# Optimization experiments

Measured on AMD Instinct MI355X. Metric: run time of the kernel, lower is better.

Reference implementation:

```python
import jax, jax.numpy as jnp
import numpy as np

NODE_DIM = 256
EDGE_DIM = 64
TIME_DIM = 1024
HEADS = 8
HEAD_DIM = NODE_DIM // HEADS
MLP = 2
BS, N = 32, 48
BN = BS * N
E = BS * N * (N - 1)


def _lin(k, fin, fout):
    return jax.random.normal(k, (fin, fout), dtype=jnp.float32) / np.sqrt(fin)


def _edge_index():
    idx = np.arange(N)
    src, dst = np.meshgrid(idx, idx, indexing='ij')
    m = src != dst
    src, dst = src[m], dst[m]              # [N*(N-1)] per graph
    offs = (np.arange(BS) * N)[:, None]
    row = (offs + src[None, :]).reshape(-1)
    col = (offs + dst[None, :]).reshape(-1)
    return jnp.asarray(np.stack([row, col]), dtype=jnp.int32)


def setup_inputs() -> dict:
    key = jax.random.key(0)
    ks = jax.random.split(key, 32)
    d = {
        'pos': jax.random.normal(ks[0], (BN, 3), jnp.float32),
        'h': jax.random.normal(ks[1], (BN, NODE_DIM), jnp.float32),
        'edge_attr': jax.random.normal(ks[2], (E, EDGE_DIM), jnp.float32),
        'node_mask': jnp.ones((BN, 1), jnp.float32),
        'node_time_emb': jax.random.normal(ks[3], (BN, TIME_DIM), jnp.float32),
        'edge_time_emb': jax.random.normal(ks[4], (E, TIME_DIM), jnp.float32),
        'edge_index': _edge_index(),
        # edge_emb: Linear(edge_dim+1 -> edge_dim)
        'W_ee': _lin(ks[5], EDGE_DIM + 1, EDGE_DIM), 'b_ee': jnp.zeros((EDGE_DIM,)),
        # AdaLN time MLPs (SiLU -> Linear)
        'W_nt': _lin(ks[6], TIME_DIM, 6 * NODE_DIM), 'b_nt': jnp.zeros((6 * NODE_DIM,)),
        'W_et': _lin(ks[7], TIME_DIM, 6 * EDGE_DIM), 'b_et': jnp.zeros((6 * EDGE_DIM,)),
        # Trans_Layer sparse attention
        'Wq': _lin(ks[8], NODE_DIM, NODE_DIM), 'bq': jnp.zeros((NODE_DIM,)),
        'Wk': _lin(ks[9], NODE_DIM, NODE_DIM), 'bk': jnp.zeros((NODE_DIM,)),
        'Wv': _lin(ks[10], NODE_DIM, NODE_DIM), 'bv': jnp.zeros((NODE_DIM,)),
        'We0': _lin(ks[11], EDGE_DIM, NODE_DIM),
        'We1': _lin(ks[12], EDGE_DIM, NODE_DIM),
        'W_n2e': _lin(ks[13], NODE_DIM, EDGE_DIM), 'b_n2e': jnp.zeros((EDGE_DIM,)),
        # node FFN
        'W_ff1': _lin(ks[14], NODE_DIM, MLP * NODE_DIM), 'b_ff1': jnp.zeros((MLP * NODE_DIM,)),
        'W_ff2': _lin(ks[15], MLP * NODE_DIM, NODE_DIM), 'b_ff2': jnp.zeros((NODE_DIM,)),
        # edge FFN
        'W_ff3': _lin(ks[16], EDGE_DIM, MLP * EDGE_DIM), 'b_ff3': jnp.zeros((MLP * EDGE_DIM,)),
        'W_ff4': _lin(ks[17], MLP * EDGE_DIM, EDGE_DIM), 'b_ff4': jnp.zeros((EDGE_DIM,)),
        # CondEquiUpdate
        'coors_scale': jnp.full((1,), 0.01, jnp.float32),
        'W_ut': _lin(ks[18], TIME_DIM, 2 * NODE_DIM), 'b_ut': jnp.zeros((2 * NODE_DIM,)),
        'W_ui': _lin(ks[19], 2 * NODE_DIM + EDGE_DIM + 1, NODE_DIM), 'b_ui': jnp.zeros((NODE_DIM,)),
        'W_uc1': _lin(ks[20], NODE_DIM, NODE_DIM), 'b_uc1': jnp.zeros((NODE_DIM,)),
        'W_uc2': _lin(ks[21], NODE_DIM, 1),
    }
    return d


def _ln(x):  # LayerNorm, no affine, eps=1e-6
    m = x.mean(-1, keepdims=True)
    v = ((x - m) ** 2).mean(-1, keepdims=True)
    return (x - m) * jax.lax.rsqrt(v + 1e-6)


def _modulate(x, shift, scale):
    return x * (1 + scale) + shift


def _block(pos, h, edge_attr, node_mask, node_time_emb, edge_time_emb, edge_index,
           W_ee, b_ee, W_nt, b_nt, W_et, b_et, Wq, bq, Wk, bk, Wv, bv, We0, We1,
           W_n2e, b_n2e, W_ff1, b_ff1, W_ff2, b_ff2, W_ff3, b_ff3, W_ff4, b_ff4,
           coors_scale, W_ut, b_ut, W_ui, b_ui, W_uc1, b_uc1, W_uc2):
    row, col = edge_index[0], edge_index[1]  # row = source j, col = target i
    diff = pos[row] - pos[col]                              # [E,3]
    dist = jnp.sqrt(jnp.sum(diff * diff, -1, keepdims=True) + 1e-12)  # [E,1]
    ea = jnp.concatenate([dist, edge_attr], -1) @ W_ee + b_ee

    nt = jax.nn.silu(node_time_emb) @ W_nt + b_nt
    n_sh_msa, n_sc_msa, n_g_msa, n_sh_mlp, n_sc_mlp, n_g_mlp = jnp.split(nt, 6, axis=1)
    et = jax.nn.silu(edge_time_emb) @ W_et + b_et
    e_sh_msa, e_sc_msa, e_g_msa, e_sh_mlp, e_sc_mlp, e_g_mlp = jnp.split(et, 6, axis=1)

    hh = _modulate(_ln(h), n_sh_msa, n_sc_msa)
    ea = _modulate(_ln(ea), e_sh_msa, e_sc_msa)

    # sparse multi-head attention over edges (Trans_Layer)
    q = (hh @ Wq + bq).reshape(BN, HEADS, HEAD_DIM)
    k = (hh @ Wk + bk).reshape(BN, HEADS, HEAD_DIM)
    v = (hh @ Wv + bv).reshape(BN, HEADS, HEAD_DIM)
    e0 = (ea @ We0).reshape(E, HEADS, HEAD_DIM)
    e1 = (ea @ We1).reshape(E, HEADS, HEAD_DIM)
    alpha = jnp.sum(q[col] * k[row] * e0, -1) / np.sqrt(HEAD_DIM)  # [E,H]
    mx = jax.ops.segment_max(alpha, col, num_segments=BN)
    ex = jnp.exp(alpha - mx[col])
    den = jax.ops.segment_sum(ex, col, num_segments=BN)
    att = ex / (den[col] + 1e-16)
    msg = v[row] * e1 * att[:, :, None]
    h_node = jax.ops.segment_sum(msg, col, num_segments=BN).reshape(BN, NODE_DIM)

    h_edge = (h_node[row] + h_node[col]) @ W_n2e + b_n2e

    h_node = h + n_g_msa * h_node
    h_node = _modulate(_ln(h_node), n_sh_mlp, n_sc_mlp) * node_mask
    ff = jax.nn.silu(h_node @ W_ff1 + b_ff1) @ W_ff2 + b_ff2
    h_out = (h_node + n_g_mlp * ff) * node_mask

    h_e = edge_attr + e_g_msa * h_edge
    h_e = _modulate(_ln(h_e), e_sh_mlp, e_sc_mlp)
    ffe = jax.nn.silu(h_e @ W_ff3 + b_ff3) @ W_ff4 + b_ff4
    h_edge_out = h_e + e_g_mlp * ffe

    # CondEquiUpdate: equivariant coordinate update
    h_input = jnp.concatenate([h_out[row], h_out[col], h_edge_out, dist], -1)
    nrm = jnp.linalg.norm(diff, axis=-1, keepdims=True)
    cdiff = diff / jnp.clip(nrm, 1e-8) * coors_scale        # CoorsNorm(scale_init=0.01)
    t_shift, t_scale = jnp.split(jax.nn.silu(edge_time_emb) @ W_ut + b_ut, 2, axis=1)
    inv = _modulate(_ln(h_input @ W_ui + b_ui), t_shift, t_scale)
    inv = jnp.tanh(jax.nn.silu(inv @ W_uc1 + b_uc1) @ W_uc2)  # [E,1]
    trans = cdiff * inv
    pos_out = pos + jax.ops.segment_sum(trans, row, num_segments=BN)
    return h_out, h_edge_out, pos_out


def reference(pos, h, edge_attr, node_mask, node_time_emb, edge_time_emb, edge_index,
              W_ee, b_ee, W_nt, b_nt, W_et, b_et, Wq, bq, Wk, bk, Wv, bv, We0, We1,
              W_n2e, b_n2e, W_ff1, b_ff1, W_ff2, b_ff2, W_ff3, b_ff3, W_ff4, b_ff4,
              coors_scale, W_ut, b_ut, W_ui, b_ui, W_uc1, b_uc1, W_uc2):
    return _block(pos, h, edge_attr, node_mask, node_time_emb, edge_time_emb, edge_index,
                  W_ee, b_ee, W_nt, b_nt, W_et, b_et, Wq, bq, Wk, bk, Wv, bv, We0, We1,
                  W_n2e, b_n2e, W_ff1, b_ff1, W_ff2, b_ff2, W_ff3, b_ff3, W_ff4, b_ff4,
                  coors_scale, W_ut, b_ut, W_ui, b_ui, W_uc1, b_uc1, W_uc2)
```

## Files before the change

kernel.cpp:

```cpp
#include <hip/hip_runtime.h>

typedef unsigned short u16;
typedef __attribute__((ext_vector_type(4))) u16 u16x4;
typedef __attribute__((ext_vector_type(8))) u16 u16x8;
typedef __attribute__((ext_vector_type(8))) short s16x8;
typedef __attribute__((ext_vector_type(4))) float f32x4;

#define E_CNT 72192
#define BN_CNT 1536
#define EPG 2256

__device__ __forceinline__ float b2f(u16 u) {
    union { unsigned int i; float f; } x; x.i = ((unsigned int)u) << 16; return x.f;
}
__device__ __forceinline__ u16 f2b(float f) {
    union { float f; unsigned int i; } x; x.f = f;
    unsigned int r = x.i + 0x7fffu + ((x.i >> 16) & 1u);
    return (u16)(r >> 16);
}
__device__ __forceinline__ float siluf(float x) { return x / (1.f + expf(-x)); }

__device__ __forceinline__ void gll16(const void* g, void* l) {
    __builtin_amdgcn_global_load_lds(
        (const __attribute__((address_space(1))) void*)g,
        (__attribute__((address_space(3))) void*)l, 16, 0, 0);
}

__device__ __forceinline__ float wave_ln64(float x) {
    float s = x;
    #pragma unroll
    for (int off = 1; off < 64; off <<= 1) s += __shfl_xor(s, off);
    float mean = s * 0.015625f;
    float d = x - mean;
    float v2 = d * d;
    #pragma unroll
    for (int off = 1; off < 64; off <<= 1) v2 += __shfl_xor(v2, off);
    return d * rsqrtf(v2 * 0.015625f + 1e-6f);
}

__device__ __forceinline__ float block_ln256(float x) {
    __shared__ float tmp[4];
    int t = threadIdx.x;
    float s = x;
    #pragma unroll
    for (int off = 1; off < 64; off <<= 1) s += __shfl_xor(s, off);
    if ((t & 63) == 0) tmp[t >> 6] = s;
    __syncthreads();
    float mean = (tmp[0] + tmp[1] + tmp[2] + tmp[3]) * (1.f / 256.f);
    float d = x - mean;
    float v2 = d * d;
    #pragma unroll
    for (int off = 1; off < 64; off <<= 1) v2 += __shfl_xor(v2, off);
    __syncthreads();
    if ((t & 63) == 0) tmp[t >> 6] = v2;
    __syncthreads();
    float var = (tmp[0] + tmp[1] + tmp[2] + tmp[3]) * (1.f / 256.f);
    return d * rsqrtf(var + 1e-6f);
}

template<int ACT, int OUTBF>
__global__ __launch_bounds__(256) void k_gemm(
    const u16* __restrict__ A, const u16* __restrict__ Bt,
    const float* __restrict__ bias, void* __restrict__ C,
    int M, int N, int K)
{
    __shared__ u16 As[64][40];
    __shared__ u16 Bs[64][40];
    int bn0 = blockIdx.x * 64, bm0 = blockIdx.y * 64;
    int t = threadIdx.x;
    int lane = t & 63, wave = t >> 6;
    int wm = wave >> 1, wn = wave & 1;
    int lr = t >> 2, lc = (t & 3) * 8;
    f32x4 acc[2][2] = {};
    const u16* Ap = A + (size_t)(bm0 + lr) * K + lc;
    const u16* Bp = Bt + (size_t)(bn0 + lr) * K + lc;
    int fr = lane & 15, fk = (lane >> 4) * 8;
    for (int k0 = 0; k0 < K; k0 += 32) {
        *(u16x8*)&As[lr][lc] = *(const u16x8*)(Ap + k0);
        *(u16x8*)&Bs[lr][lc] = *(const u16x8*)(Bp + k0);
        __syncthreads();
        s16x8 a0 = *(const s16x8*)&As[wm * 32 + fr][fk];
        s16x8 a1 = *(const s16x8*)&As[wm * 32 + 16 + fr][fk];
        s16x8 b0 = *(const s16x8*)&Bs[wn * 32 + fr][fk];
        s16x8 b1 = *(const s16x8*)&Bs[wn * 32 + 16 + fr][fk];
        acc[0][0] = __builtin_amdgcn_mfma_f32_16x16x32_bf16(a0, b0, acc[0][0], 0, 0, 0);
        acc[0][1] = __builtin_amdgcn_mfma_f32_16x16x32_bf16(a0, b1, acc[0][1], 0, 0, 0);
        acc[1][0] = __builtin_amdgcn_mfma_f32_16x16x32_bf16(a1, b0, acc[1][0], 0, 0, 0);
        acc[1][1] = __builtin_amdgcn_mfma_f32_16x16x32_bf16(a1, b1, acc[1][1], 0, 0, 0);
        __syncthreads();
    }
    int cIn = lane & 15, r4 = (lane >> 4) * 4;
    #pragma unroll
    for (int i = 0; i < 2; i++)
    #pragma unroll
    for (int j = 0; j < 2; j++) {
        int col = bn0 + wn * 32 + j * 16 + cIn;
        float bv = bias ? bias[col] : 0.f;
        #pragma unroll
        for (int r = 0; r < 4; r++) {
            int rowg = bm0 + wm * 32 + i * 16 + r4 + r;
            float vv = acc[i][j][r] + bv;
            if (ACT == 1) vv = siluf(vv);
            if (OUTBF) ((u16*)C)[(size_t)rowg * N + col] = f2b(vv);
            else       ((float*)C)[(size_t)rowg * N + col] = vv;
        }
    }
}

template<int ACT, int OUTBF>
__global__ __launch_bounds__(256) void k_gemm128(
    const u16* __restrict__ A, const u16* __restrict__ Bt,
    const float* __restrict__ bias, void* __restrict__ C,
    int M, int N, int K)
{
    __shared__ u16 As[3][128 * 32];
    __shared__ u16 Bs[3][128 * 32];
    const int t = threadIdx.x;
    const int lane = t & 63, wv = t >> 6;
    const int wm = wv >> 1, wn = wv & 1;
    const int nwg = gridDim.x * gridDim.y;
    const int orig = blockIdx.y * gridDim.x + blockIdx.x;
    const int q8 = nwg >> 3, r8 = nwg & 7;
    const int xcd = orig & 7, lin = orig >> 3;
    const int wgid = (xcd < r8 ? xcd * (q8 + 1) : r8 * (q8 + 1) + (xcd - r8) * q8) + lin;
    const int bxs = wgid % gridDim.x, bys = wgid / gridDim.x;
    const int bn0 = bxs * 128, bm0 = bys * 128;
    const int srow = t >> 2;
    const int scol = ((t & 3) ^ ((t >> 3) & 3)) * 8;
    const u16* Ap = A + (size_t)(bm0 + srow) * K + scol;
    const u16* Bp = Bt + (size_t)(bn0 + srow) * K + scol;
    const size_t rstep = (size_t)64 * K;
    const int woff = wv * 16 * 32;
    const int fr = lane & 15;
    const int fkc = (((lane >> 4) ^ ((fr >> 1) & 3)) * 8);
    f32x4 acc[4][4] = {};
    const int NT = K >> 5;

    auto STAGE = [&](int b, int ko) {
        gll16(Ap + ko, &As[b][woff]);
        gll16(Ap + ko + rstep, &As[b][woff + 64 * 32]);
        gll16(Bp + ko, &Bs[b][woff]);
        gll16(Bp + ko + rstep, &Bs[b][woff + 64 * 32]);
    };
    auto COMPUTE = [&](int b) {
        const u16* aBase = &As[b][wm * 64 * 32];
        const u16* bBase = &Bs[b][wn * 64 * 32];
        s16x8 af[4], bfr[4];
        #pragma unroll
        for (int m = 0; m < 4; m++) af[m] = *(const s16x8*)&aBase[(m * 16 + fr) * 32 + fkc];
        #pragma unroll
        for (int n = 0; n < 4; n++) bfr[n] = *(const s16x8*)&bBase[(n * 16 + fr) * 32 + fkc];
        #pragma unroll
        for (int m = 0; m < 4; m++)
        #pragma unroll
        for (int n = 0; n < 4; n++)
            acc[m][n] = __builtin_amdgcn_mfma_f32_16x16x32_bf16(af[m], bfr[n], acc[m][n], 0, 0, 0);
    };

    STAGE(0, 0);
    if (NT > 1) STAGE(1, 32);
    int cur = 0;
    for (int tt = 0; tt < NT; tt++) {
        if (tt + 2 < NT) STAGE((cur + 2) % 3, (tt + 2) * 32);
        __builtin_amdgcn_sched_barrier(0);
        int ahead = NT - 1 - tt; if (ahead > 2) ahead = 2;
        if (ahead == 2)      asm volatile("s_waitcnt vmcnt(8)" ::: "memory");
        else if (ahead == 1) asm volatile("s_waitcnt vmcnt(4)" ::: "memory");
        else                 asm volatile("s_waitcnt vmcnt(0)" ::: "memory");
        __builtin_amdgcn_sched_barrier(0);
        __builtin_amdgcn_s_barrier();
        COMPUTE(cur);
        __builtin_amdgcn_s_barrier();
        __builtin_amdgcn_sched_barrier(0);
        cur = (cur + 1) % 3;
    }

    const int cIn = lane & 15, r4 = (lane >> 4) * 4;
    #pragma unroll
    for (int n = 0; n < 4; n++) {
        int col = bn0 + wn * 64 + n * 16 + cIn;
        float bv = bias ? bias[col] : 0.f;
        #pragma unroll
        for (int m = 0; m < 4; m++) {
            #pragma unroll
            for (int r = 0; r < 4; r++) {
                int rowg = bm0 + wm * 64 + m * 16 + r4 + r;
                float vv = acc[m][n][r] + bv;
                if (ACT == 1) vv = siluf(vv);
                if (OUTBF) ((u16*)C)[(size_t)rowg * N + col] = f2b(vv);
                else       ((float*)C)[(size_t)rowg * N + col] = vv;
            }
        }
    }
}

struct ConvJob { const float* W; u16* Wt; int ldw, k0, n0, K, nc_start; };
struct CopyJob { const float* src; float* dst; int n; };
struct BatchArgs { ConvJob cj[17]; CopyJob cp[5]; int conv_blocks; };

__global__ __launch_bounds__(256) void k_prep(BatchArgs a)
{
    int b = blockIdx.x;
    if (b < a.conv_blocks) {
        int j = 0;
        #pragma unroll 1
        while (j + 1 < 17 && a.cj[j + 1].nc_start <= b) ++j;
        const ConvJob J = a.cj[j];
        int n = b - J.nc_start;
        for (int k = threadIdx.x; k < J.K; k += 256)
            J.Wt[(size_t)n * J.K + k] = f2b(J.W[(size_t)(J.k0 + k) * J.ldw + J.n0 + n]);
    } else {
        int c = b - a.conv_blocks;
        const CopyJob C = a.cp[c];
        for (int i = threadIdx.x; i < C.n; i += 256) C.dst[i] = C.src[i];
    }
}

__global__ void k_silu_bf(const float* __restrict__ in, u16* __restrict__ out, int n4)
{
    int i = blockIdx.x * 256 + threadIdx.x;
    int stride = gridDim.x * 256;
    for (; i < n4; i += stride) {
        f32x4 v = *(const f32x4*)(in + (size_t)i * 4);
        u16x4 o;
        #pragma unroll
        for (int j = 0; j < 4; j++) o[j] = f2b(siluf(v[j]));
        *(u16x4*)(out + (size_t)i * 4) = o;
    }
}

__global__ __launch_bounds__(256) void k_edge_pre(
    const float* __restrict__ pos, const float* __restrict__ edge_attr,
    const int* __restrict__ ei, const float* __restrict__ W_ee,
    const float* __restrict__ b_ee, const float* __restrict__ coors_scale,
    const u16* __restrict__ etf,
    u16* __restrict__ ea_mod, float* __restrict__ dist, float* __restrict__ cdiff)
{
    __shared__ float Ws[65][64];
    int t = threadIdx.x;
    for (int i = t; i < 65 * 64; i += 256) Ws[i >> 6][i & 63] = W_ee[i];
    __syncthreads();
    int l = t & 63;
    float bee = b_ee[l];
    float cscale = coors_scale[0];
    for (int g = 0; g < 16; g++) {
        int e = blockIdx.x * 64 + g * 4 + (t >> 6);
        int row = ei[e], col = ei[E_CNT + e];
        float d0 = pos[row * 3 + 0] - pos[col * 3 + 0];
        float d1 = pos[row * 3 + 1] - pos[col * 3 + 1];
        float d2 = pos[row * 3 + 2] - pos[col * 3 + 2];
        float ssq = d0 * d0 + d1 * d1 + d2 * d2;
        float dst = sqrtf(ssq + 1e-12f);
        float nrm = sqrtf(ssq);
        float cs = cscale / fmaxf(nrm, 1e-8f);
        if (l == 0) {
            dist[e] = dst;
            cdiff[e * 3 + 0] = d0 * cs; cdiff[e * 3 + 1] = d1 * cs; cdiff[e * 3 + 2] = d2 * cs;
        }
        float attr = edge_attr[(size_t)e * 64 + l];
        float acc = dst * Ws[0][l];
        for (int f = 0; f < 64; f++) acc += __shfl(attr, f) * Ws[1 + f][l];
        acc += bee;
        float y = wave_ln64(acc);
        const u16* ep = etf + (size_t)e * 896;
        float m = y * (1.f + b2f(ep[64 + l])) + b2f(ep[l]);
        ea_mod[(size_t)e * 64 + l] = f2b(m);
    }
}

__global__ __launch_bounds__(256) void k_node_hh(
    const float* __restrict__ h, const float* __restrict__ nt, u16* __restrict__ hh)
{
    int n = blockIdx.x, c = threadIdx.x;
    float x = h[(size_t)n * 256 + c];
    float y = block_ln256(x);
    float m = y * (1.f + nt[(size_t)n * 1536 + 256 + c]) + nt[(size_t)n * 1536 + c];
    hh[(size_t)n * 256 + c] = f2b(m);
}

__global__ __launch_bounds__(256) void k_agg(
    const float* __restrict__ qkv, const u16* __restrict__ e01,
    float* __restrict__ hnode, u16* __restrict__ hnode_bf)
{
    int n = blockIdx.x;
    int b = n / 48, i = n % 48;
    int t = threadIdx.x;
    __shared__ float qs[8][33];
    __shared__ float att[47][8];
    __shared__ float mxs[8], dens[8];
    __shared__ int elist[47], slist[47];
    qs[t >> 5][t & 31] = qkv[(size_t)n * 768 + t];
    if (t < 47) {
        int s = t + (t >= i ? 1 : 0);
        slist[t] = s;
        elist[t] = b * EPG + s * 47 + (i < s ? i : i - 1);
    }
    __syncthreads();
    for (int idx = t; idx < 376; idx += 256) {
        int j = idx >> 3, hh = idx & 7;
        int src = b * 48 + slist[j];
        int e = elist[j];
        const float* kp = qkv + (size_t)src * 768 + 256 + hh * 32;
        const u16* ep = e01 + (size_t)e * 512 + hh * 32;
        float p = 0.f;
        #pragma unroll
        for (int d = 0; d < 32; d++) p += qs[hh][d] * kp[d] * b2f(ep[d]);
        att[j][hh] = p * 0.17677669529663687f;
    }
    __syncthreads();
    if (t < 8) {
        float m = -1e30f;
        for (int j = 0; j < 47; j++) m = fmaxf(m, att[j][t]);
        float den = 0.f;
        for (int j = 0; j < 47; j++) den += expf(att[j][t] - m);
        mxs[t] = m; dens[t] = den + 1e-16f;
    }
    __syncthreads();
    for (int idx = t; idx < 376; idx += 256) {
        int j = idx >> 3, hh = idx & 7;
        att[j][hh] = expf(att[j][hh] - mxs[hh]) / dens[hh];
    }
    __syncthreads();
    int c = t, hh = t >> 5;
    float acc = 0.f;
    for (int j = 0; j < 47; j++) {
        int src = b * 48 + slist[j];
        int e = elist[j];
        acc += att[j][hh] * qkv[(size_t)src * 768 + 512 + c] * b2f(e01[(size_t)e * 512 + 256 + c]);
    }
    hnode[(size_t)n * 256 + c] = acc;
    hnode_bf[(size_t)n * 256 + c] = f2b(acc);
}

__global__ __launch_bounds__(256) void k_node_mod(
    const float* __restrict__ h, const float* __restrict__ hnode_raw,
    const float* __restrict__ nt, const float* __restrict__ mask,
    float* __restrict__ hmod, u16* __restrict__ hmod_bf)
{
    int n = blockIdx.x, c = threadIdx.x;
    float x = h[(size_t)n * 256 + c] + nt[(size_t)n * 1536 + 512 + c] * hnode_raw[(size_t)n * 256 + c];
    float y = block_ln256(x);
    float m = (y * (1.f + nt[(size_t)n * 1536 + 1024 + c]) + nt[(size_t)n * 1536 + 768 + c]) * mask[n];
    hmod[(size_t)n * 256 + c] = m;
    hmod_bf[(size_t)n * 256 + c] = f2b(m);
}

__global__ void k_hout(const float* __restrict__ hmod, const float* __restrict__ ff2,
                       const float* __restrict__ nt, const float* __restrict__ mask,
                       float* __restrict__ out, u16* __restrict__ hout_bf)
{
    int i = blockIdx.x * 256 + threadIdx.x;
    if (i >= BN_CNT * 256) return;
    int n = i >> 8, c = i & 255;
    float v = (hmod[i] + nt[(size_t)n * 1536 + 1280 + c] * ff2[i]) * mask[n];
    out[i] = v;
    hout_bf[i] = f2b(v);
}

__global__ __launch_bounds__(256) void k_edge_mod(
    const float* __restrict__ Q1, const float* __restrict__ b_n2e,
    const float* __restrict__ edge_attr, const int* __restrict__ ei,
    const u16* __restrict__ etf, float* __restrict__ hemod, u16* __restrict__ hemod_bf)
{
    int e = blockIdx.x * 4 + (threadIdx.x >> 6);
    int l = threadIdx.x & 63;
    int row = ei[e], col = ei[E_CNT + e];
    float hedge = Q1[(size_t)row * 64 + l] + Q1[(size_t)col * 64 + l] + b_n2e[l];
    const u16* ep = etf + (size_t)e * 896;
    float x = edge_attr[(size_t)e * 64 + l] + b2f(ep[128 + l]) * hedge;
    float y = wave_ln64(x);
    float m = y * (1.f + b2f(ep[256 + l])) + b2f(ep[192 + l]);
    hemod[(size_t)e * 64 + l] = m;
    hemod_bf[(size_t)e * 64 + l] = f2b(m);
}

__global__ void k_edge_out(const float* __restrict__ hemod, const float* __restrict__ ff4,
                           const u16* __restrict__ etf,
                           float* __restrict__ out2, u16* __restrict__ heout_bf)
{
    size_t i = (size_t)blockIdx.x * 256 + threadIdx.x;
    if (i >= (size_t)E_CNT * 64) return;
    int e = (int)(i >> 6), c = (int)(i & 63);
    float v = hemod[i] + b2f(etf[(size_t)e * 896 + 320 + c]) * ff4[i];
    out2[i] = v;
    heout_bf[i] = f2b(v);
}

__global__ __launch_bounds__(256) void k_inv_pre(
    const float* __restrict__ p12,
    const u16* __restrict__ P3, const float* __restrict__ dist,
    const float* __restrict__ W_ui, const float* __restrict__ b_ui,
    const int* __restrict__ ei, const u16* __restrict__ etf, u16* __restrict__ invmod)
{
    int e = blockIdx.x, c = threadIdx.x;
    int row = ei[e], col = ei[E_CNT + e];
    float x = p12[(size_t)row * 512 + c] + p12[(size_t)col * 512 + 256 + c]
            + b2f(P3[(size_t)e * 256 + c]) + dist[e] * W_ui[576 * 256 + c] + b_ui[c];
    float y = block_ln256(x);
    const u16* ep = etf + (size_t)e * 896;
    float m = y * (1.f + b2f(ep[640 + c])) + b2f(ep[384 + c]);
    invmod[(size_t)e * 256 + c] = f2b(m);
}

__global__ __launch_bounds__(256) void k_inv(const u16* __restrict__ uc1,
                                             const float* __restrict__ W_uc2,
                                             float* __restrict__ inv)
{
    int e = blockIdx.x * 4 + (threadIdx.x >> 6);
    int l = threadIdx.x & 63;
    u16x4 v = *(const u16x4*)(uc1 + (size_t)e * 256 + l * 4);
    const float* w = W_uc2 + l * 4;
    float s = b2f(v[0]) * w[0] + b2f(v[1]) * w[1] + b2f(v[2]) * w[2] + b2f(v[3]) * w[3];
    #pragma unroll
    for (int off = 1; off < 64; off <<= 1) s += __shfl_xor(s, off);
    if (l == 0) inv[e] = tanhf(s);
}

__global__ void k_pos(const float* __restrict__ pos, const float* __restrict__ cdiff,
                      const float* __restrict__ inv, float* __restrict__ out3)
{
    int n = blockIdx.x * 256 + threadIdx.x;
    if (n >= BN_CNT) return;
    int b = n / 48, s = n % 48;
    int e0 = b * EPG + s * 47;
    float a0 = 0.f, a1 = 0.f, a2 = 0.f;
    for (int j = 0; j < 47; j++) {
        float f = inv[e0 + j];
        a0 += cdiff[(size_t)(e0 + j) * 3 + 0] * f;
        a1 += cdiff[(size_t)(e0 + j) * 3 + 1] * f;
        a2 += cdiff[(size_t)(e0 + j) * 3 + 2] * f;
    }
    out3[n * 3 + 0] = pos[n * 3 + 0] + a0;
    out3[n * 3 + 1] = pos[n * 3 + 1] + a1;
    out3[n * 3 + 2] = pos[n * 3 + 2] + a2;
}

extern "C" void kernel_launch(void* const* d_in, const int* in_sizes, int n_in,
                              void* d_out, int out_size, void* d_ws, size_t ws_size,
                              hipStream_t stream)
{
    (void)in_sizes; (void)n_in; (void)out_size; (void)ws_size;
    const float* pos       = (const float*)d_in[0];
    const float* h         = (const float*)d_in[1];
    const float* edge_attr = (const float*)d_in[2];
    const float* node_mask = (const float*)d_in[3];
    const float* nte       = (const float*)d_in[4];
    const float* ete       = (const float*)d_in[5];
    const int*   ei        = (const int*)d_in[6];
    const float* W_ee = (const float*)d_in[7];  const float* b_ee = (const float*)d_in[8];
    const float* W_nt = (const float*)d_in[9];  const float* b_nt = (const float*)d_in[10];
    const float* W_et = (const float*)d_in[11]; const float* b_et = (const float*)d_in[12];
    const float* Wq  = (const float*)d_in[13];  const float* bq  = (const float*)d_in[14];
    const float* Wk  = (const float*)d_in[15];  const float* bk  = (const float*)d_in[16];
    const float* Wv  = (const float*)d_in[17];  const float* bv  = (const float*)d_in[18];
    const float* We0 = (const float*)d_in[19];  const float* We1 = (const float*)d_in[20];
    const float* W_n2e = (const float*)d_in[21]; const float* b_n2e = (const float*)d_in[22];
    const float* W_ff1 = (const float*)d_in[23]; const float* b_ff1 = (const float*)d_in[24];
    const float* W_ff2 = (const float*)d_in[25]; const float* b_ff2 = (const float*)d_in[26];
    const float* W_ff3 = (const float*)d_in[27]; const float* b_ff3 = (const float*)d_in[28];
    const float* W_ff4 = (const float*)d_in[29]; const float* b_ff4 = (const float*)d_in[30];
    const float* coors_scale = (const float*)d_in[31];
    const float* W_ut = (const float*)d_in[32]; const float* b_ut = (const float*)d_in[33];
    const float* W_ui = (const float*)d_in[34]; const float* b_ui = (const float*)d_in[35];
    const float* W_uc1 = (const float*)d_in[36]; const float* b_uc1 = (const float*)d_in[37];
    const float* W_uc2 = (const float*)d_in[38];

    const size_t E = E_CNT;
    char* ws = (char*)d_ws;
    size_t off = 0;
    auto AL = [&](size_t b) { size_t o = off; off += (b + 255) & ~(size_t)255; return o; };

    size_t o_wtcat  = AL(896 * 1024 * 2);
    size_t o_wtnt   = AL(1536 * 1024 * 2);
    size_t o_wtqkv  = AL(768 * 256 * 2);
    size_t o_wte01  = AL(512 * 64 * 2);
    size_t o_wtn2e  = AL(64 * 256 * 2);
    size_t o_wtff1  = AL(512 * 256 * 2), o_wtff2 = AL(256 * 512 * 2);
    size_t o_wtff3  = AL(128 * 64 * 2),  o_wtff4 = AL(64 * 128 * 2);
    size_t o_wtuiab = AL(512 * 256 * 2);
    size_t o_wtuic  = AL(256 * 64 * 2),  o_wtuc1 = AL(256 * 256 * 2);
    size_t o_bias896 = AL(896 * 4);
    size_t o_bias768 = AL(768 * 4);
    size_t o_reg1 = AL(E * 1024 * 2);
    size_t o_etf  = AL(E * 896 * 2);
    size_t o_ntes = AL(1536 * 1024 * 2);
    size_t o_ntf  = AL((size_t)1536 * 1536 * 4);
    size_t o_eamod = AL(E * 64 * 2);
    size_t o_dist = AL(E * 4), o_cdiff = AL(E * 12);
    size_t o_qkv  = AL(1536 * 768 * 4);
    size_t o_reg3 = AL(E * 512 * 2);
    size_t o_hnode = AL(1536 * 256 * 4), o_hnodebf = AL(1536 * 256 * 2);
    size_t o_q1 = AL(1536 * 64 * 4);
    size_t o_hh = AL(1536 * 256 * 2);
    size_t o_hmod = AL(1536 * 256 * 4), o_hmodbf = AL(1536 * 256 * 2);
    size_t o_ff1 = AL(1536 * 512 * 2), o_ff2 = AL(1536 * 256 * 4);
    size_t o_houtbf = AL(1536 * 256 * 2);
    size_t o_hemod = AL(E * 64 * 4), o_hemodbf = AL(E * 64 * 2);
    size_t o_p12 = AL(1536 * 512 * 4);
    size_t o_inv = AL(E * 4);
    size_t o_etes = o_reg1;
    size_t o_p3 = o_reg1;
    size_t o_invmod = o_reg1 + E * 256 * 2;
    size_t o_uc1o = o_reg1 + E * 256 * 4;
    size_t o_e01 = o_reg3;
    size_t o_ffem = o_reg3;
    size_t o_ff4o = o_reg3 + E * 128 * 2;
    size_t o_heoutbf = o_reg3 + E * 128 * 2 + E * 64 * 4;

    #define WSU(o) ((u16*)(ws + (o)))
    #define WSF(o) ((float*)(ws + (o)))

    {
        BatchArgs a;
        int s = 0; int j = 0;
        auto add = [&](const float* W, u16* Wt, int ldw, int k0, int n0, int K, int NC) {
            a.cj[j++] = ConvJob{W, Wt, ldw, k0, n0, K, s}; s += NC;
        };
        add(W_et, WSU(o_wtcat), 384, 0, 0, 1024, 384);
        add(W_ut, WSU(o_wtcat) + (size_t)384 * 1024, 512, 0, 0, 1024, 512);
        add(W_nt, WSU(o_wtnt), 1536, 0, 0, 1024, 1536);
        add(Wq, WSU(o_wtqkv), 256, 0, 0, 256, 256);
        add(Wk, WSU(o_wtqkv) + (size_t)256 * 256, 256, 0, 0, 256, 256);
        add(Wv, WSU(o_wtqkv) + (size_t)512 * 256, 256, 0, 0, 256, 256);
        add(We0, WSU(o_wte01), 256, 0, 0, 64, 256);
        add(We1, WSU(o_wte01) + (size_t)256 * 64, 256, 0, 0, 64, 256);
        add(W_n2e, WSU(o_wtn2e), 64, 0, 0, 256, 64);
        add(W_ff1, WSU(o_wtff1), 512, 0, 0, 256, 512);
        add(W_ff2, WSU(o_wtff2), 256, 0, 0, 512, 256);
        add(W_ff3, WSU(o_wtff3), 128, 0, 0, 64, 128);
        add(W_ff4, WSU(o_wtff4), 64, 0, 0, 128, 64);
        add(W_ui, WSU(o_wtuiab), 256, 0, 0, 256, 256);
        add(W_ui, WSU(o_wtuiab) + (size_t)256 * 256, 256, 256, 0, 256, 256);
        add(W_ui, WSU(o_wtuic), 256, 512, 0, 64, 256);
        add(W_uc1, WSU(o_wtuc1), 256, 0, 0, 256, 256);
        a.conv_blocks = s;
        a.cp[0] = CopyJob{b_et, WSF(o_bias896), 384};
        a.cp[1] = CopyJob{b_ut, WSF(o_bias896) + 384, 512};
        a.cp[2] = CopyJob{bq, WSF(o_bias768), 256};
        a.cp[3] = CopyJob{bk, WSF(o_bias768) + 256, 256};
        a.cp[4] = CopyJob{bv, WSF(o_bias768) + 512, 256};
        k_prep<<<s + 5, 256, 0, stream>>>(a);
    }

    k_silu_bf<<<2048, 256, 0, stream>>>(ete, WSU(o_etes), (int)(E * 1024 / 4));
    k_silu_bf<<<1024, 256, 0, stream>>>(nte, WSU(o_ntes), 1536 * 1024 / 4);

    k_gemm128<0, 1><<<dim3(7, 564), 256, 0, stream>>>(WSU(o_etes), WSU(o_wtcat), WSF(o_bias896), WSU(o_etf), E_CNT, 896, 1024);
    k_gemm<0, 0><<<dim3(24, 24), 256, 0, stream>>>(WSU(o_ntes), WSU(o_wtnt), b_nt, WSF(o_ntf), 1536, 1536, 1024);

    k_edge_pre<<<1128, 256, 0, stream>>>(pos, edge_attr, ei, W_ee, b_ee, coors_scale,
                                         WSU(o_etf), WSU(o_eamod), WSF(o_dist), WSF(o_cdiff));

    k_node_hh<<<1536, 256, 0, stream>>>(h, WSF(o_ntf), WSU(o_hh));
    k_gemm<0, 0><<<dim3(12, 24), 256, 0, stream>>>(WSU(o_hh), WSU(o_wtqkv), WSF(o_bias768), WSF(o_qkv), 1536, 768, 256);
    k_gemm128<0, 1><<<dim3(4, 564), 256, 0, stream>>>(WSU(o_eamod), WSU(o_wte01), nullptr, WSU(o_e01), E_CNT, 512, 64);
    k_agg<<<1536, 256, 0, stream>>>(WSF(o_qkv), WSU(o_e01), WSF(o_hnode), WSU(o_hnodebf));

    k_gemm<0, 0><<<dim3(1, 24), 256, 0, stream>>>(WSU(o_hnodebf), WSU(o_wtn2e), nullptr, WSF(o_q1), 1536, 64, 256);

    k_node_mod<<<1536, 256, 0, stream>>>(h, WSF(o_hnode), WSF(o_ntf), node_mask, WSF(o_hmod), WSU(o_hmodbf));
    k_gemm<1, 1><<<dim3(8, 24), 256, 0, stream>>>(WSU(o_hmodbf), WSU(o_wtff1), b_ff1, WSU(o_ff1), 1536, 512, 256);
    k_gemm<0, 0><<<dim3(4, 24), 256, 0, stream>>>(WSU(o_ff1), WSU(o_wtff2), b_ff2, WSF(o_ff2), 1536, 256, 512);
    k_hout<<<1536, 256, 0, stream>>>(WSF(o_hmod), WSF(o_ff2), WSF(o_ntf), node_mask, (float*)d_out, WSU(o_houtbf));

    k_edge_mod<<<18048, 256, 0, stream>>>(WSF(o_q1), b_n2e, edge_attr, ei, WSU(o_etf), WSF(o_hemod), WSU(o_hemodbf));
    k_gemm128<1, 1><<<dim3(1, 564), 256, 0, stream>>>(WSU(o_hemodbf), WSU(o_wtff3), b_ff3, WSU(o_ffem), E_CNT, 128, 64);
    k_gemm<0, 0><<<dim3(1, 1128), 256, 0, stream>>>(WSU(o_ffem), WSU(o_wtff4), b_ff4, WSF(o_ff4o), E_CNT, 64, 128);
    k_edge_out<<<18048, 256, 0, stream>>>(WSF(o_hemod), WSF(o_ff4o), WSU(o_etf),
                                          (float*)d_out + 393216, WSU(o_heoutbf));

    k_gemm<0, 0><<<dim3(8, 24), 256, 0, stream>>>(WSU(o_houtbf), WSU(o_wtuiab), nullptr, WSF(o_p12), 1536, 512, 256);
    k_gemm128<0, 1><<<dim3(2, 564), 256, 0, stream>>>(WSU(o_heoutbf), WSU(o_wtuic), nullptr, WSU(o_p3), E_CNT, 256, 64);
    k_inv_pre<<<E_CNT, 256, 0, stream>>>(WSF(o_p12), WSU(o_p3), WSF(o_dist),
                                         W_ui, b_ui, ei, WSU(o_etf), WSU(o_invmod));
    k_gemm128<1, 1><<<dim3(2, 564), 256, 0, stream>>>(WSU(o_invmod), WSU(o_wtuc1), b_uc1, WSU(o_uc1o), E_CNT, 256, 256);
    k_inv<<<18048, 256, 0, stream>>>(WSU(o_uc1o), W_uc2, WSF(o_inv));
    k_pos<<<6, 256, 0, stream>>>(pos, WSF(o_cdiff), WSF(o_inv), (float*)d_out + 393216 + E_CNT * 64);

    #undef WSU
    #undef WSF
}
```

Measured before the change: 758.5 us.

## Add 256x256-tile GEMM kernel with 512 threads for large edge GEMMs

Adds a new bf16 MFMA GEMM kernel using 256x256 output tiles, 8 waves per block and a triple-buffered LDS pipeline. The four large edge-dimension GEMMs switch to it from the 128-tile kernel, which raises data reuse per block and cuts global traffic. For the N=896 GEMM the padded fourth column tile is masked on store, and the weight workspace is grown to 1024 rows so the out-of-range B loads stay in bounds. The larger tile uses about 96KB of LDS and many accumulator registers, so only one block fits per CU, and the N=896 case spends compute on the padded columns.

```diff
diff --git a/kernel.cpp b/kernel.cpp
--- a/kernel.cpp
+++ b/kernel.cpp
@@ -189,6 +189,95 @@
                 if (ACT == 1) vv = siluf(vv);
                 if (OUTBF) ((u16*)C)[(size_t)rowg * N + col] = f2b(vv);
                 else       ((float*)C)[(size_t)rowg * N + col] = vv;
+            }
+        }
+    }
+}
+
+template<int ACT, int OUTBF>
+__global__ __launch_bounds__(512, 1) void k_gemm256(
+    const u16* __restrict__ A, const u16* __restrict__ Bt,
+    const float* __restrict__ bias, void* __restrict__ C,
+    int M, int N, int K)
+{
+    __shared__ u16 As[3][256 * 32];
+    __shared__ u16 Bs[3][256 * 32];
+    const int t = threadIdx.x;
+    const int lane = t & 63, wv = t >> 6;
+    const int wm = wv >> 2, wn = wv & 3;
+    const int nwg = gridDim.x * gridDim.y;
+    const int orig = blockIdx.y * gridDim.x + blockIdx.x;
+    const int q8 = nwg >> 3, r8 = nwg & 7;
+    const int xcd = orig & 7, lin = orig >> 3;
+    const int wgid = (xcd < r8 ? xcd * (q8 + 1) : r8 * (q8 + 1) + (xcd - r8) * q8) + lin;
+    const int bn0 = (wgid % gridDim.x) * 256, bm0 = (wgid / gridDim.x) * 256;
+    const int r0 = t >> 2;
+    const int c0 = ((t & 3) ^ ((t >> 3) & 3)) * 8;
+    const u16* A0 = A + (size_t)(bm0 + r0) * K + c0;
+    const u16* B0 = Bt + (size_t)(bn0 + r0) * K + c0;
+    const size_t rstep = (size_t)128 * K;
+    const int w0 = (wv * 64) * 8;
+    const int w1 = (512 + wv * 64) * 8;
+    const int fr = lane & 15;
+    const int fkc = (((lane >> 4) ^ ((fr >> 1) & 3)) * 8);
+    f32x4 acc[8][4] = {};
+    const int NT = K >> 5;
+
+    auto STAGE = [&](int b, int ko) {
+        gll16(A0 + ko, &As[b][w0]);
+        gll16(A0 + ko + rstep, &As[b][w1]);
+        gll16(B0 + ko, &Bs[b][w0]);
+        gll16(B0 + ko + rstep, &Bs[b][w1]);
+    };
+    auto COMPUTE = [&](int b) {
+        s16x8 af[8], bfr[4];
+        #pragma unroll
+        for (int m = 0; m < 8; m++)
+            af[m] = *(const s16x8*)&As[b][(wm * 128 + m * 16 + fr) * 32 + fkc];
+        #pragma unroll
+        for (int n = 0; n < 4; n++)
+            bfr[n] = *(const s16x8*)&Bs[b][(wn * 64 + n * 16 + fr) * 32 + fkc];
+        #pragma unroll
+        for (int m = 0; m < 8; m++)
+        #pragma unroll
+        for (int n = 0; n < 4; n++)
+            acc[m][n] = __builtin_amdgcn_mfma_f32_16x16x32_bf16(af[m], bfr[n], acc[m][n], 0, 0, 0);
+    };
+
+    STAGE(0, 0);
+    if (NT > 1) STAGE(1, 32);
+    int cur = 0;
+    for (int tt = 0; tt < NT; tt++) {
+        if (tt + 2 < NT) STAGE((cur + 2) % 3, (tt + 2) * 32);
+        __builtin_amdgcn_sched_barrier(0);
+        int ahead = NT - 1 - tt; if (ahead > 2) ahead = 2;
+        if (ahead == 2)      asm volatile("s_waitcnt vmcnt(8)" ::: "memory");
+        else if (ahead == 1) asm volatile("s_waitcnt vmcnt(4)" ::: "memory");
+        else                 asm volatile("s_waitcnt vmcnt(0)" ::: "memory");
+        __builtin_amdgcn_sched_barrier(0);
+        __builtin_amdgcn_s_barrier();
+        COMPUTE(cur);
+        __builtin_amdgcn_s_barrier();
+        __builtin_amdgcn_sched_barrier(0);
+        cur = (cur + 1) % 3;
+    }
+
+    const int cIn = lane & 15, r4 = (lane >> 4) * 4;
+    #pragma unroll
+    for (int n = 0; n < 4; n++) {
+        int col = bn0 + wn * 64 + n * 16 + cIn;
+        if (col < N) {
+            float bv = bias ? bias[col] : 0.f;
+            #pragma unroll
+            for (int m = 0; m < 8; m++) {
+                #pragma unroll
+                for (int r = 0; r < 4; r++) {
+                    int rowg = bm0 + wm * 128 + m * 16 + r4 + r;
+                    float vv = acc[m][n][r] + bv;
+                    if (ACT == 1) vv = siluf(vv);
+                    if (OUTBF) ((u16*)C)[(size_t)rowg * N + col] = f2b(vv);
+                    else       ((float*)C)[(size_t)rowg * N + col] = vv;
+                }
             }
         }
     }
@@ -470,7 +559,7 @@
     size_t off = 0;
     auto AL = [&](size_t b) { size_t o = off; off += (b + 255) & ~(size_t)255; return o; };
 
-    size_t o_wtcat  = AL(896 * 1024 * 2);
+    size_t o_wtcat  = AL((size_t)1024 * 1024 * 2);
     size_t o_wtnt   = AL(1536 * 1024 * 2);
     size_t o_wtqkv  = AL(768 * 256 * 2);
     size_t o_wte01  = AL(512 * 64 * 2);
@@ -545,7 +634,8 @@
     k_silu_bf<<<2048, 256, 0, stream>>>(ete, WSU(o_etes), (int)(E * 1024 / 4));
     k_silu_bf<<<1024, 256, 0, stream>>>(nte, WSU(o_ntes), 1536 * 1024 / 4);
 
-    k_gemm128<0, 1><<<dim3(7, 564), 256, 0, stream>>>(WSU(o_etes), WSU(o_wtcat), WSF(o_bias896), WSU(o_etf), E_CNT, 896, 1024);
+    k_gemm256<0, 1><<<dim3(4, 282), 512, 0, stream>>>(
+        WSU(o_etes), WSU(o_wtcat), WSF(o_bias896), WSU(o_etf), E_CNT, 896, 1024);
     k_gemm<0, 0><<<dim3(24, 24), 256, 0, stream>>>(WSU(o_ntes), WSU(o_wtnt), b_nt, WSF(o_ntf), 1536, 1536, 1024);
 
     k_edge_pre<<<1128, 256, 0, stream>>>(pos, edge_attr, ei, W_ee, b_ee, coors_scale,
@@ -553,7 +643,8 @@
 
     k_node_hh<<<1536, 256, 0, stream>>>(h, WSF(o_ntf), WSU(o_hh));
     k_gemm<0, 0><<<dim3(12, 24), 256, 0, stream>>>(WSU(o_hh), WSU(o_wtqkv), WSF(o_bias768), WSF(o_qkv), 1536, 768, 256);
-    k_gemm128<0, 1><<<dim3(4, 564), 256, 0, stream>>>(WSU(o_eamod), WSU(o_wte01), nullptr, WSU(o_e01), E_CNT, 512, 64);
+    k_gemm256<0, 1><<<dim3(2, 282), 512, 0, stream>>>(
+        WSU(o_eamod), WSU(o_wte01), nullptr, WSU(o_e01), E_CNT, 512, 64);
     k_agg<<<1536, 256, 0, stream>>>(WSF(o_qkv), WSU(o_e01), WSF(o_hnode), WSU(o_hnodebf));
 
     k_gemm<0, 0><<<dim3(1, 24), 256, 0, stream>>>(WSU(o_hnodebf), WSU(o_wtn2e), nullptr, WSF(o_q1), 1536, 64, 256);
@@ -570,10 +661,12 @@
                                           (float*)d_out + 393216, WSU(o_heoutbf));
 
     k_gemm<0, 0><<<dim3(8, 24), 256, 0, stream>>>(WSU(o_houtbf), WSU(o_wtuiab), nullptr, WSF(o_p12), 1536, 512, 256);
-    k_gemm128<0, 1><<<dim3(2, 564), 256, 0, stream>>>(WSU(o_heoutbf), WSU(o_wtuic), nullptr, WSU(o_p3), E_CNT, 256, 64);
+    k_gemm256<0, 1><<<dim3(1, 282), 512, 0, stream>>>(
+        WSU(o_heoutbf), WSU(o_wtuic), nullptr, WSU(o_p3), E_CNT, 256, 64);
     k_inv_pre<<<E_CNT, 256, 0, stream>>>(WSF(o_p12), WSU(o_p3), WSF(o_dist),
                                          W_ui, b_ui, ei, WSU(o_etf), WSU(o_invmod));
-    k_gemm128<1, 1><<<dim3(2, 564), 256, 0, stream>>>(WSU(o_invmod), WSU(o_wtuc1), b_uc1, WSU(o_uc1o), E_CNT, 256, 256);
+    k_gemm256<1, 1><<<dim3(1, 282), 512, 0, stream>>>(
+        WSU(o_invmod), WSU(o_wtuc1), b_uc1, WSU(o_uc1o), E_CNT, 256, 256);
     k_inv<<<18048, 256, 0, stream>>>(WSU(o_uc1o), W_uc2, WSF(o_inv));
     k_pos<<<6, 256, 0, stream>>>(pos, WSF(o_cdiff), WSF(o_inv), (float*)d_out + 393216 + E_CNT * 64);
 
```

Result: slower. 874.0 us (+15.2%).
